# Kernel tuning notes

Measured on AMD Instinct MI355X. Metric: run time of the kernel, lower is better.

Reference implementation:

```python
import jax, jax.numpy as jnp
import numpy as np

CODE_NUM = 12288
GRAPH = 128      # graph_size: embedding width / GRU input
HIDDEN = 128     # GRU hidden = t_output_size = time_size (required by scatter/broadcast)
ATT = 64         # t_attention_size


def setup_inputs() -> dict:
    key = jax.random.key(0)
    ks = jax.random.split(key, 20)
    s = 0.05
    # disjoint 3-way membership masks (m1/m2/m3), some codes in no set
    cat = jax.random.randint(ks[0], (CODE_NUM,), 0, 4)
    divided = jax.nn.one_hot(cat, 4, dtype=jnp.int32)[:, :3]
    return {
        "interval": jnp.asarray(3.5, jnp.float32),
        "co_embeddings": jax.random.normal(ks[1], (CODE_NUM, GRAPH), jnp.float32),
        "no_embeddings": jax.random.normal(ks[2], (CODE_NUM, GRAPH), jnp.float32),
        "unrelated_embeddings": jax.random.normal(ks[3], (CODE_NUM, GRAPH), jnp.float32),
        "hidden_state": jax.random.normal(ks[4], (CODE_NUM, HIDDEN), jnp.float32),
        "divided": divided,
        # GRUCell params (torch layout: [3H, in], gates r|z|n)
        "W_ih": jax.random.normal(ks[5], (3 * HIDDEN, GRAPH), jnp.float32) * s,
        "W_hh": jax.random.normal(ks[6], (3 * HIDDEN, HIDDEN), jnp.float32) * s,
        "b_ih": jax.random.normal(ks[7], (3 * HIDDEN,), jnp.float32) * s,
        "b_hh": jax.random.normal(ks[8], (3 * HIDDEN,), jnp.float32) * s,
        # SingleHeadAttentionLayer params
        "Wq": jax.random.normal(ks[9], (ATT, GRAPH), jnp.float32) * s,
        "bq": jax.random.normal(ks[10], (ATT,), jnp.float32) * s,
        "Wk": jax.random.normal(ks[11], (ATT, GRAPH), jnp.float32) * s,
        "bk": jax.random.normal(ks[12], (ATT,), jnp.float32) * s,
        "Wv": jax.random.normal(ks[13], (HIDDEN, GRAPH), jnp.float32) * s,
        "bv": jax.random.normal(ks[14], (HIDDEN,), jnp.float32) * s,
        # time_layer: Linear(1, time_size)
        "Wt": jax.random.normal(ks[15], (HIDDEN, 1), jnp.float32) * s,
        "bt": jax.random.normal(ks[16], (HIDDEN,), jnp.float32) * s,
        "t": 1,
        "is_last": 0,
    }


def _gru_cell(x, h, W_ih, W_hh, b_ih, b_hh):
    gi = x @ W_ih.T + b_ih          # [N, 3H]
    gh = h @ W_hh.T + b_hh          # [N, 3H]
    i_r, i_z, i_n = jnp.split(gi, 3, axis=-1)
    h_r, h_z, h_n = jnp.split(gh, 3, axis=-1)
    r = jax.nn.sigmoid(i_r + h_r)
    z = jax.nn.sigmoid(i_z + h_z)
    n = jnp.tanh(i_n + r * h_n)
    return (1.0 - z) * n + z * h


def reference(interval, co_embeddings, no_embeddings, unrelated_embeddings,
              hidden_state, divided, W_ih, W_hh, b_ih, b_hh,
              Wq, bq, Wk, bk, Wv, bv, Wt, bt, t, is_last):
    dt = co_embeddings.dtype
    # time feature: tanh(Linear(1/log(interval + e)))
    x_t = 1.0 / jnp.log(interval + jnp.e)                       # scalar
    time_features = jnp.tanh(x_t * Wt[:, 0] + bt)               # [H]

    if is_last:
        out = _gru_cell(co_embeddings, hidden_state, W_ih, W_hh, b_ih, b_hh)
        return (out + time_features, None)

    m1 = divided[:, 0] > 0
    m2 = divided[:, 1] > 0
    m3 = divided[:, 2] > 0
    m23 = m2 | m3
    NEG = jnp.finfo(dt).min

    # --- m1 branch: GRUCell is row-wise, so compute on all rows and mask ---
    h_gru = _gru_cell(co_embeddings, hidden_state, W_ih, W_hh, b_ih, b_hh)  # [N, H]
    output_m1 = jnp.max(jnp.where(m1[:, None], h_gru, NEG), axis=0)        # [H]

    # --- m2/m3 branch: attention over the m23 subset (mask-based, order-free)
    # query rows: m2 -> no_embeddings, m3 -> unrelated_embeddings
    q_full = jnp.where(m2[:, None], no_embeddings, unrelated_embeddings)   # [N, G]
    Q = q_full @ Wq.T + bq                                                 # [N, A]
    K = co_embeddings @ Wk.T + bk                                          # [N, A]
    V = co_embeddings @ Wv.T + bv                                          # [N, H]
    scores = (Q @ K.T) / jnp.sqrt(jnp.asarray(ATT, dt))                    # [N, N]
    scores = jnp.where(m23[None, :], scores, NEG)                          # keys restricted to m23
    attn = jax.nn.softmax(scores, axis=-1)
    h_att = jnp.tanh(attn @ V)                                             # [N, H]
    output_m23 = jnp.max(jnp.where(m23[:, None], h_att, NEG), axis=0)      # [H]

    # scatter: m2/m3 rows written after m1 rows (m23 takes precedence)
    h_new = jnp.where(m23[:, None], h_att,
                      jnp.where(m1[:, None], h_gru, jnp.zeros((), dt)))

    output = jnp.maximum(output_m1, output_m23)
    return (output + time_features, h_new)
```

## Files before the change

### kernel.cpp

```cpp
#include <hip/hip_runtime.h>
#include <hip/hip_bf16.h>
#include <math.h>

#define N_CODES 12288
#define G 128
#define H 128
#define ATT 64
#define NEGF (-3.4028234663852886e38f)
#define NSEG 8
#define QT 64
#define NQT (N_CODES / QT)
#define QMAX 7168

typedef __attribute__((ext_vector_type(8))) short bf16x8;
typedef __attribute__((ext_vector_type(4))) float f32x4;
typedef __hip_bfloat16 bf16;
#define MFMA16(a, b, c) __builtin_amdgcn_mfma_f32_16x16x32_bf16(a, b, c, 0, 0, 0)

struct __align__(16) Ws {
  int n1;
  int n23;
  int pad_[2];
  int idx1[N_CODES];
  int rows23[N_CODES];
  int flags23[N_CODES];
  unsigned maxu[128];
  float tf[128];
  float lseg[NSEG * QMAX];
  float bqkv[256];
  float b2[512];
  bf16 Wqkv[16 * 4 * 64 * 8];
  bf16 W2[32 * 8 * 64 * 8];
  bf16 Qb[(size_t)N_CODES * ATT];
  bf16 Kf[(size_t)N_CODES * ATT];
  bf16 Vf[(size_t)N_CODES * H];
  bf16 Oseg[(size_t)NSEG * QMAX * H];
};

__device__ inline uint2 pack4(float4 v) {
  union { bf16 b[4]; uint2 u; } cv;
  cv.b[0] = __float2bfloat16(v.x);
  cv.b[1] = __float2bfloat16(v.y);
  cv.b[2] = __float2bfloat16(v.z);
  cv.b[3] = __float2bfloat16(v.w);
  return cv.u;
}

__device__ inline float bf2f(short s) {
  union { unsigned u; float f; } c;
  c.u = ((unsigned)(unsigned short)s) << 16;
  return c.f;
}

__device__ inline unsigned fkey(float f) {
  unsigned b = __float_as_uint(f);
  return (b & 0x80000000u) ? ~b : (b | 0x80000000u);
}
__device__ inline float funkey(unsigned u) {
  unsigned b = (u & 0x80000000u) ? (u & 0x7fffffffu) : ~u;
  return __uint_as_float(b);
}

__global__ void k_setup(const int* __restrict__ divided,
                        const float* __restrict__ Wq, const float* __restrict__ bq,
                        const float* __restrict__ Wk, const float* __restrict__ bk,
                        const float* __restrict__ Wv, const float* __restrict__ bv,
                        const float* __restrict__ W_ih, const float* __restrict__ W_hh,
                        const float* __restrict__ b_ih, const float* __restrict__ b_hh,
                        const float* __restrict__ interval, const float* __restrict__ Wt,
                        const float* __restrict__ bt, Ws* ws) {
  int bid = blockIdx.x;
  int t = threadIdx.x;
  if (bid < 48) {
    int r = bid * 256 + t;
    int m1 = divided[r * 3 + 0] > 0;
    int m2 = divided[r * 3 + 1] > 0;
    int m3 = divided[r * 3 + 2] > 0;
    if (m1) {
      int p = atomicAdd(&ws->n1, 1);
      ws->idx1[p] = r;
    }
    if (m2 | m3) {
      int p = atomicAdd(&ws->n23, 1);
      ws->rows23[p] = r;
      ws->flags23[p] = m2;
    }
    return;
  }
  if (bid < 176) {
    int idx = (bid - 48) * 256 + t;
    int c = idx >> 7, k = idx & 127;
    float v;
    if (c < 64) v = Wq[c * G + k] * 0.125f;
    else if (c < 128) v = Wk[(c - 64) * G + k];
    else v = Wv[(c - 128) * G + k];
    int NB = c >> 4, lo = c & 15, ks = k >> 5, hi = (k >> 3) & 3, j = k & 7;
    ws->Wqkv[((NB * 4 + ks) * 64 + hi * 16 + lo) * 8 + j] = __float2bfloat16(v);
    return;
  }
  if (bid < 688) {
    int idx = (bid - 176) * 256 + t;
    int c = idx >> 8, k = idx & 255;
    int g = c >> 7, d = c & 127;
    float v = 0.f;
    if (g == 0) v = (k < 128) ? W_ih[d * G + k] : W_hh[d * H + (k - 128)];
    else if (g == 1) v = (k < 128) ? W_ih[(128 + d) * G + k] : W_hh[(128 + d) * H + (k - 128)];
    else if (g == 2) v = (k < 128) ? W_ih[(256 + d) * G + k] : 0.f;
    else v = (k < 128) ? 0.f : W_hh[(256 + d) * H + (k - 128)];
    int NB = c >> 4, lo = c & 15, ks = k >> 5, hi = (k >> 3) & 3, j = k & 7;
    ws->W2[((NB * 8 + ks) * 64 + hi * 16 + lo) * 8 + j] = __float2bfloat16(v);
    return;
  }
  if (t < 128) {
    float xt = 1.0f / logf(interval[0] + 2.718281828459045f);
    ws->tf[t] = tanhf(xt * Wt[t] + bt[t]);
    ws->maxu[t] = 0u;
  }
  for (int i = t; i < 768; i += 256) {
    if (i < 256) {
      float v;
      if (i < 64) v = bq[i] * 0.125f;
      else if (i < 128) v = bk[i - 64];
      else v = bv[i - 128];
      ws->bqkv[i] = v;
    } else {
      int c = i - 256;
      int g = c >> 7, d = c & 127;
      float v;
      if (g == 0) v = b_ih[d] + b_hh[d];
      else if (g == 1) v = b_ih[128 + d] + b_hh[128 + d];
      else if (g == 2) v = b_ih[256 + d];
      else v = b_hh[256 + d];
      ws->b2[c] = v;
    }
  }
}

__launch_bounds__(256)
__global__ void k_mm(const float* __restrict__ co, const float* __restrict__ no_e,
                     const float* __restrict__ un_e, const float* __restrict__ hs,
                     Ws* ws, float* __restrict__ h_new) {
  __shared__ __align__(16) bf16 sm[8704];
  int bid = blockIdx.x;
  int t = threadIdx.x;
  int w = t >> 6, lane = t & 63, lo = lane & 15, hi = lane >> 4;

  if (bid < 384) {
    int n23 = ws->n23;
    int q0 = bid * 32;
    if (q0 >= n23) return;
    bf16(*Aq)[136] = (bf16(*)[136])sm;
    bf16(*Ac)[136] = (bf16(*)[136])(sm + 4352);
    for (int it = 0; it < 4; ++it) {
      int idx = it * 256 + t;
      int rr = idx >> 5, c4 = idx & 31;
      uint2 pq = {0, 0}, pc = {0, 0};
      int p = q0 + rr;
      if (p < n23) {
        int row = ws->rows23[p];
        const float* srcq = ws->flags23[p] ? no_e : un_e;
        pq = pack4(*(const float4*)&srcq[(size_t)row * G + c4 * 4]);
        pc = pack4(*(const float4*)&co[(size_t)row * G + c4 * 4]);
      }
      *(uint2*)&Aq[rr][c4 * 4] = pq;
      *(uint2*)&Ac[rr][c4 * 4] = pc;
    }
    __syncthreads();
    const bf16(*At)[136] = (w == 0) ? Aq : Ac;
    f32x4 acc[2][4];
#pragma unroll
    for (int mf = 0; mf < 2; ++mf)
#pragma unroll
      for (int nb = 0; nb < 4; ++nb) acc[mf][nb] = (f32x4){0.f, 0.f, 0.f, 0.f};
#pragma unroll
    for (int ks = 0; ks < 4; ++ks) {
      bf16x8 af0 = *(const bf16x8*)&At[lo][ks * 32 + hi * 8];
      bf16x8 af1 = *(const bf16x8*)&At[16 + lo][ks * 32 + hi * 8];
#pragma unroll
      for (int nb = 0; nb < 4; ++nb) {
        bf16x8 bfr = *(const bf16x8*)&ws->Wqkv[(((w * 4 + nb) * 4 + ks) * 64 + lane) * 8];
        acc[0][nb] = MFMA16(af0, bfr, acc[0][nb]);
        acc[1][nb] = MFMA16(af1, bfr, acc[1][nb]);
      }
    }
#pragma unroll
    for (int mf = 0; mf < 2; ++mf) {
#pragma unroll
      for (int nb = 0; nb < 4; ++nb) {
        int c = w * 64 + nb * 16 + lo;
        float bias = ws->bqkv[c];
#pragma unroll
        for (int r = 0; r < 4; ++r) {
          int p = q0 + mf * 16 + hi * 4 + r;
          if (p >= n23) continue;
          bf16 bv16 = __float2bfloat16(acc[mf][nb][r] + bias);
          if (c < 64) {
            ws->Qb[(size_t)p * ATT + c] = bv16;
          } else if (c < 128) {
            int d = c - 64;
            ws->Kf[(((p >> 4) * 2 + (d >> 5)) * 64 + ((d >> 3) & 3) * 16 + (p & 15)) * 8 + (d & 7)] = bv16;
          } else {
            int d = c - 128;
            ws->Vf[((((p >> 6) * 8 + (d >> 4)) * 2 + ((p >> 5) & 1)) * 64 + ((p >> 3) & 3) * 16 + (d & 15)) * 8 + (p & 7)] = bv16;
          }
        }
      }
    }
  } else {
    int n1 = ws->n1;
    int q0 = (bid - 384) * 32;
    if (q0 >= n1) return;
    bf16(*A2)[264] = (bf16(*)[264])sm;
    for (int it = 0; it < 8; ++it) {
      int idx = it * 256 + t;
      int rr = idx >> 6, c4 = idx & 63;
      uint2 pk = {0, 0};
      int p = q0 + rr;
      if (p < n1) {
        int row = ws->idx1[p];
        float4 v = (c4 < 32) ? *(const float4*)&co[(size_t)row * G + c4 * 4]
                             : *(const float4*)&hs[(size_t)row * H + (c4 - 32) * 4];
        pk = pack4(v);
      }
      *(uint2*)&A2[rr][c4 * 4] = pk;
    }
    __syncthreads();
    f32x4 acc[2][8];
#pragma unroll
    for (int mf = 0; mf < 2; ++mf)
#pragma unroll
      for (int x = 0; x < 8; ++x) acc[mf][x] = (f32x4){0.f, 0.f, 0.f, 0.f};
#pragma unroll
    for (int ks = 0; ks < 8; ++ks) {
      bf16x8 af0 = *(const bf16x8*)&A2[lo][ks * 32 + hi * 8];
      bf16x8 af1 = *(const bf16x8*)&A2[16 + lo][ks * 32 + hi * 8];
#pragma unroll
      for (int g = 0; g < 4; ++g) {
#pragma unroll
        for (int nb2 = 0; nb2 < 2; ++nb2) {
          int NB = g * 8 + w * 2 + nb2;
          bf16x8 bfr = *(const bf16x8*)&ws->W2[((NB * 8 + ks) * 64 + lane) * 8];
          acc[0][g * 2 + nb2] = MFMA16(af0, bfr, acc[0][g * 2 + nb2]);
          acc[1][g * 2 + nb2] = MFMA16(af1, bfr, acc[1][g * 2 + nb2]);
        }
      }
    }
    float mx2[2] = {NEGF, NEGF};
#pragma unroll
    for (int mf = 0; mf < 2; ++mf) {
#pragma unroll
      for (int nb2 = 0; nb2 < 2; ++nb2) {
        int d = w * 32 + nb2 * 16 + lo;
        float br = ws->b2[d], bz = ws->b2[128 + d], bin_ = ws->b2[256 + d], bhn = ws->b2[384 + d];
#pragma unroll
        for (int r = 0; r < 4; ++r) {
          int p = q0 + mf * 16 + hi * 4 + r;
          if (p >= n1) continue;
          int row = ws->idx1[p];
          float rs = acc[mf][0 + nb2][r] + br;
          float zs = acc[mf][2 + nb2][r] + bz;
          float in_ = acc[mf][4 + nb2][r] + bin_;
          float hn = acc[mf][6 + nb2][r] + bhn;
          float rg = 1.f / (1.f + __expf(-rs));
          float zg = 1.f / (1.f + __expf(-zs));
          float ng = tanhf(in_ + rg * hn);
          float h0 = hs[(size_t)row * H + d];
          float hv = (1.f - zg) * ng + zg * h0;
          h_new[(size_t)row * H + d] = hv;
          mx2[nb2] = fmaxf(mx2[nb2], hv);
        }
      }
    }
#pragma unroll
    for (int nb2 = 0; nb2 < 2; ++nb2) {
      float m = mx2[nb2];
      m = fmaxf(m, __shfl_xor(m, 16));
      m = fmaxf(m, __shfl_xor(m, 32));
      if (hi == 0) atomicMax(&ws->maxu[w * 32 + nb2 * 16 + lo], fkey(m));
    }
  }
}

__launch_bounds__(256)
__global__ void k_attn(const Ws* __restrict__ ws, Ws* __restrict__ wso) {
  int n23 = ws->n23;
  int bid = blockIdx.x;
  int q0 = (bid % NQT) * QT;
  int seg = bid / NQT;
  if (q0 >= n23) return;
  int segk = (((n23 + NSEG - 1) / NSEG) + 63) & ~63;
  int s0 = seg * segk;
  int t = threadIdx.x;
  if (s0 >= n23) {
    for (int idx = t; idx < QT * 32; idx += 256) {
      int q = q0 + (idx >> 5);
      if (q < n23) {
        uint2 z2 = {0, 0};
        *(uint2*)&wso->Oseg[((size_t)seg * QMAX + q) * H + (idx & 31) * 4] = z2;
      }
    }
    if (t < QT && q0 + t < n23) wso->lseg[seg * QMAX + q0 + t] = 0.f;
    return;
  }
  int send = min(s0 + segk, n23);

  int w = t >> 6, lane = t & 63, lo = lane & 15, hi = lane >> 4;

  __shared__ bf16 Pl[64][72];

  bf16x8 qf[4][2];
#pragma unroll
  for (int qsub = 0; qsub < 4; ++qsub)
#pragma unroll
    for (int s = 0; s < 2; ++s)
      qf[qsub][s] =
          *(const bf16x8*)&ws->Qb[(size_t)(q0 + qsub * 16 + lo) * ATT + s * 32 + hi * 8];

  f32x4 acc[2][4];
#pragma unroll
  for (int ddl = 0; ddl < 2; ++ddl)
#pragma unroll
    for (int qsub = 0; qsub < 4; ++qsub) acc[ddl][qsub] = (f32x4){0.f, 0.f, 0.f, 0.f};
  float lacc = 0.f;

  for (int c0 = s0; c0 < send; c0 += 64) {
    int kb = (c0 >> 4) + w;
    bf16x8 kf0 = *(const bf16x8*)&ws->Kf[((size_t)(kb * 2 + 0) * 64 + lane) * 8];
    bf16x8 kf1 = *(const bf16x8*)&ws->Kf[((size_t)(kb * 2 + 1) * 64 + lane) * 8];
    bool kv = (c0 + w * 16 + lo) < send;
#pragma unroll
    for (int qsub = 0; qsub < 4; ++qsub) {
      f32x4 s_ = {0.f, 0.f, 0.f, 0.f};
      s_ = MFMA16(qf[qsub][0], kf0, s_);
      s_ = MFMA16(qf[qsub][1], kf1, s_);
#pragma unroll
      for (int r = 0; r < 4; ++r) {
        float p = kv ? __expf(s_[r]) : 0.f;
        Pl[qsub * 16 + hi * 4 + r][w * 16 + lo] = __float2bfloat16(p);
      }
    }
    __syncthreads();

    int kc = c0 >> 6;
#pragma unroll
    for (int s = 0; s < 2; ++s) {
      bf16x8 pf[4];
#pragma unroll
      for (int qsub = 0; qsub < 4; ++qsub)
        pf[qsub] = *(const bf16x8*)&Pl[qsub * 16 + lo][s * 32 + hi * 8];
#pragma unroll
      for (int ddl = 0; ddl < 2; ++ddl) {
        bf16x8 vf =
            *(const bf16x8*)&ws->Vf[((size_t)(kc * 16 + (w * 2 + ddl) * 2 + s) * 64 + lane) * 8];
#pragma unroll
        for (int qsub = 0; qsub < 4; ++qsub) acc[ddl][qsub] = MFMA16(vf, pf[qsub], acc[ddl][qsub]);
      }
    }
    {
      bf16x8 pa = *(const bf16x8*)&Pl[w * 16 + lo][hi * 16];
      bf16x8 pb = *(const bf16x8*)&Pl[w * 16 + lo][hi * 16 + 8];
      float sl = 0.f;
#pragma unroll
      for (int j = 0; j < 8; ++j) sl += bf2f(pa[j]) + bf2f(pb[j]);
      sl += __shfl_xor(sl, 16);
      sl += __shfl_xor(sl, 32);
      lacc += sl;
    }
    __syncthreads();
  }

  if (hi == 0) {
    int q = q0 + w * 16 + lo;
    if (q < n23) wso->lseg[seg * QMAX + q] = lacc;
  }
#pragma unroll
  for (int qsub = 0; qsub < 4; ++qsub) {
    int q = q0 + qsub * 16 + lo;
    if (q < n23) {
#pragma unroll
      for (int ddl = 0; ddl < 2; ++ddl) {
        union { bf16 b[4]; uint2 u; } tmp;
#pragma unroll
        for (int r = 0; r < 4; ++r) tmp.b[r] = __float2bfloat16(acc[ddl][qsub][r]);
        *(uint2*)&wso->Oseg[((size_t)seg * QMAX + q) * H + w * 32 + ddl * 16 + hi * 4] = tmp.u;
      }
    }
  }
}

__global__ void k_merge(const Ws* __restrict__ ws, float* __restrict__ h_new, Ws* wso) {
  int n23 = ws->n23;
  int qb = blockIdx.x * 32;
  if (qb >= n23) return;
  int t = threadIdx.x;
  int d = t & 127, half = t >> 7;
  float mx = NEGF;
  for (int qi = 0; qi < 16; ++qi) {
    int q = qb + half * 16 + qi;
    if (q >= n23) break;
    float o = 0.f, L = 0.f;
#pragma unroll
    for (int s = 0; s < NSEG; ++s) {
      o += bf2f(((const short*)ws->Oseg)[((size_t)s * QMAX + q) * H + d]);
      L += ws->lseg[s * QMAX + q];
    }
    float h = tanhf(o / L);
    h_new[(size_t)ws->rows23[q] * H + d] = h;
    mx = fmaxf(mx, h);
  }
  __shared__ float red[256];
  red[t] = mx;
  __syncthreads();
  if (t < 128) atomicMax(&wso->maxu[t], fkey(fmaxf(red[t], red[t + 128])));
}

__global__ void k_final(const Ws* __restrict__ ws, float* __restrict__ out) {
  int h = threadIdx.x;
  out[h] = funkey(ws->maxu[h]) + ws->tf[h];
}

extern "C" void kernel_launch(void* const* d_in, const int* in_sizes, int n_in,
                              void* d_out, int out_size, void* d_ws, size_t ws_size,
                              hipStream_t stream) {
  const float* interval = (const float*)d_in[0];
  const float* co = (const float*)d_in[1];
  const float* no_e = (const float*)d_in[2];
  const float* un_e = (const float*)d_in[3];
  const float* hs = (const float*)d_in[4];
  const int* divided = (const int*)d_in[5];
  const float* W_ih = (const float*)d_in[6];
  const float* W_hh = (const float*)d_in[7];
  const float* b_ih = (const float*)d_in[8];
  const float* b_hh = (const float*)d_in[9];
  const float* Wq = (const float*)d_in[10];
  const float* bq = (const float*)d_in[11];
  const float* Wk = (const float*)d_in[12];
  const float* bk = (const float*)d_in[13];
  const float* Wv = (const float*)d_in[14];
  const float* bv = (const float*)d_in[15];
  const float* Wt = (const float*)d_in[16];
  const float* bt = (const float*)d_in[17];

  float* out = (float*)d_out;
  float* h_new = out + 128;
  Ws* ws = (Ws*)d_ws;

  hipMemsetAsync(d_out, 0, (size_t)out_size * sizeof(float), stream);
  hipMemsetAsync(ws, 0, 16, stream);

  k_setup<<<689, 256, 0, stream>>>(divided, Wq, bq, Wk, bk, Wv, bv, W_ih, W_hh, b_ih, b_hh,
                                   interval, Wt, bt, ws);
  k_mm<<<768, 256, 0, stream>>>(co, no_e, un_e, hs, ws, h_new);
  k_attn<<<NQT * NSEG, 256, 0, stream>>>(ws, ws);
  k_merge<<<QMAX / 32, 256, 0, stream>>>(ws, h_new, ws);
  k_final<<<1, 128, 0, stream>>>(ws, out);
}
```

Measured before the change: 194.6 us.

## Vectorize weight packing, shrink matmul tiles, fuse final reduction into merge

The weight-repacking setup blocks now read float4 and write packed bf16 quads, which cuts the setup grid from 689 to 209 blocks. The projection and GRU matmul blocks drop from 32 to 16 rows so more blocks share the work. The attention grid is sized by QMAX instead of N_CODES so fewer blocks exit early. Attention now computes the transposed score tile, so P is stored as packed 64-bit writes and the row sums are accumulated in registers, removing the extra LDS re-read. The k_final launch is folded into k_merge through a last-block counter, which adds a threadfence and atomic handshake.

```diff
diff --git a/kernel.cpp b/kernel.cpp
--- a/kernel.cpp
+++ b/kernel.cpp
@@ -9,8 +9,8 @@
 #define NEGF (-3.4028234663852886e38f)
 #define NSEG 8
 #define QT 64
-#define NQT (N_CODES / QT)
 #define QMAX 7168
+#define NQTA (QMAX / QT)
 
 typedef __attribute__((ext_vector_type(8))) short bf16x8;
 typedef __attribute__((ext_vector_type(4))) float f32x4;
@@ -20,7 +20,8 @@
 struct __align__(16) Ws {
   int n1;
   int n23;
-  int pad_[2];
+  int cnt;
+  int pad_;
   int idx1[N_CODES];
   int rows23[N_CODES];
   int flags23[N_CODES];
@@ -87,28 +88,35 @@
     }
     return;
   }
-  if (bid < 176) {
+  if (bid < 80) {
     int idx = (bid - 48) * 256 + t;
-    int c = idx >> 7, k = idx & 127;
-    float v;
-    if (c < 64) v = Wq[c * G + k] * 0.125f;
-    else if (c < 128) v = Wk[(c - 64) * G + k];
-    else v = Wv[(c - 128) * G + k];
+    int c = idx >> 5, k = (idx & 31) * 4;
+    float4 v;
+    if (c < 64) {
+      v = *(const float4*)&Wq[c * G + k];
+      v.x *= 0.125f; v.y *= 0.125f; v.z *= 0.125f; v.w *= 0.125f;
+    } else if (c < 128) {
+      v = *(const float4*)&Wk[(c - 64) * G + k];
+    } else {
+      v = *(const float4*)&Wv[(c - 128) * G + k];
+    }
     int NB = c >> 4, lo = c & 15, ks = k >> 5, hi = (k >> 3) & 3, j = k & 7;
-    ws->Wqkv[((NB * 4 + ks) * 64 + hi * 16 + lo) * 8 + j] = __float2bfloat16(v);
+    *(uint2*)&ws->Wqkv[((NB * 4 + ks) * 64 + hi * 16 + lo) * 8 + j] = pack4(v);
     return;
   }
-  if (bid < 688) {
-    int idx = (bid - 176) * 256 + t;
-    int c = idx >> 8, k = idx & 255;
+  if (bid < 208) {
+    int idx = (bid - 80) * 256 + t;
+    int c = idx >> 6, k = (idx & 63) * 4;
     int g = c >> 7, d = c & 127;
-    float v = 0.f;
-    if (g == 0) v = (k < 128) ? W_ih[d * G + k] : W_hh[d * H + (k - 128)];
-    else if (g == 1) v = (k < 128) ? W_ih[(128 + d) * G + k] : W_hh[(128 + d) * H + (k - 128)];
-    else if (g == 2) v = (k < 128) ? W_ih[(256 + d) * G + k] : 0.f;
-    else v = (k < 128) ? 0.f : W_hh[(256 + d) * H + (k - 128)];
+    float4 v = {0.f, 0.f, 0.f, 0.f};
+    if (g == 0) v = (k < 128) ? *(const float4*)&W_ih[d * G + k]
+                              : *(const float4*)&W_hh[d * H + (k - 128)];
+    else if (g == 1) v = (k < 128) ? *(const float4*)&W_ih[(128 + d) * G + k]
+                                   : *(const float4*)&W_hh[(128 + d) * H + (k - 128)];
+    else if (g == 2) { if (k < 128) v = *(const float4*)&W_ih[(256 + d) * G + k]; }
+    else { if (k >= 128) v = *(const float4*)&W_hh[(256 + d) * H + (k - 128)]; }
     int NB = c >> 4, lo = c & 15, ks = k >> 5, hi = (k >> 3) & 3, j = k & 7;
-    ws->W2[((NB * 8 + ks) * 64 + hi * 16 + lo) * 8 + j] = __float2bfloat16(v);
+    *(uint2*)&ws->W2[((NB * 8 + ks) * 64 + hi * 16 + lo) * 8 + j] = pack4(v);
     return;
   }
   if (t < 128) {
@@ -145,13 +153,13 @@
   int t = threadIdx.x;
   int w = t >> 6, lane = t & 63, lo = lane & 15, hi = lane >> 4;
 
-  if (bid < 384) {
+  if (bid < 448) {
     int n23 = ws->n23;
-    int q0 = bid * 32;
+    int q0 = bid * 16;
     if (q0 >= n23) return;
     bf16(*Aq)[136] = (bf16(*)[136])sm;
-    bf16(*Ac)[136] = (bf16(*)[136])(sm + 4352);
-    for (int it = 0; it < 4; ++it) {
+    bf16(*Ac)[136] = (bf16(*)[136])(sm + 2176);
+    for (int it = 0; it < 2; ++it) {
       int idx = it * 256 + t;
       int rr = idx >> 5, c4 = idx & 31;
       uint2 pq = {0, 0}, pc = {0, 0};
@@ -167,51 +175,44 @@
     }
     __syncthreads();
     const bf16(*At)[136] = (w == 0) ? Aq : Ac;
-    f32x4 acc[2][4];
-#pragma unroll
-    for (int mf = 0; mf < 2; ++mf)
-#pragma unroll
-      for (int nb = 0; nb < 4; ++nb) acc[mf][nb] = (f32x4){0.f, 0.f, 0.f, 0.f};
+    f32x4 acc[4];
+#pragma unroll
+    for (int nb = 0; nb < 4; ++nb) acc[nb] = (f32x4){0.f, 0.f, 0.f, 0.f};
 #pragma unroll
     for (int ks = 0; ks < 4; ++ks) {
-      bf16x8 af0 = *(const bf16x8*)&At[lo][ks * 32 + hi * 8];
-      bf16x8 af1 = *(const bf16x8*)&At[16 + lo][ks * 32 + hi * 8];
+      bf16x8 af = *(const bf16x8*)&At[lo][ks * 32 + hi * 8];
 #pragma unroll
       for (int nb = 0; nb < 4; ++nb) {
         bf16x8 bfr = *(const bf16x8*)&ws->Wqkv[(((w * 4 + nb) * 4 + ks) * 64 + lane) * 8];
-        acc[0][nb] = MFMA16(af0, bfr, acc[0][nb]);
-        acc[1][nb] = MFMA16(af1, bfr, acc[1][nb]);
-      }
-    }
-#pragma unroll
-    for (int mf = 0; mf < 2; ++mf) {
-#pragma unroll
-      for (int nb = 0; nb < 4; ++nb) {
-        int c = w * 64 + nb * 16 + lo;
-        float bias = ws->bqkv[c];
-#pragma unroll
-        for (int r = 0; r < 4; ++r) {
-          int p = q0 + mf * 16 + hi * 4 + r;
-          if (p >= n23) continue;
-          bf16 bv16 = __float2bfloat16(acc[mf][nb][r] + bias);
-          if (c < 64) {
-            ws->Qb[(size_t)p * ATT + c] = bv16;
-          } else if (c < 128) {
-            int d = c - 64;
-            ws->Kf[(((p >> 4) * 2 + (d >> 5)) * 64 + ((d >> 3) & 3) * 16 + (p & 15)) * 8 + (d & 7)] = bv16;
-          } else {
-            int d = c - 128;
-            ws->Vf[((((p >> 6) * 8 + (d >> 4)) * 2 + ((p >> 5) & 1)) * 64 + ((p >> 3) & 3) * 16 + (d & 15)) * 8 + (p & 7)] = bv16;
-          }
+        acc[nb] = MFMA16(af, bfr, acc[nb]);
+      }
+    }
+#pragma unroll
+    for (int nb = 0; nb < 4; ++nb) {
+      int c = w * 64 + nb * 16 + lo;
+      float bias = ws->bqkv[c];
+#pragma unroll
+      for (int r = 0; r < 4; ++r) {
+        int p = q0 + hi * 4 + r;
+        if (p >= n23) continue;
+        bf16 bv16 = __float2bfloat16(acc[nb][r] + bias);
+        if (c < 64) {
+          ws->Qb[(size_t)p * ATT + c] = bv16;
+        } else if (c < 128) {
+          int d = c - 64;
+          ws->Kf[(((p >> 4) * 2 + (d >> 5)) * 64 + ((d >> 3) & 3) * 16 + (p & 15)) * 8 + (d & 7)] = bv16;
+        } else {
+          int d = c - 128;
+          ws->Vf[((((p >> 6) * 8 + (d >> 4)) * 2 + ((p >> 5) & 1)) * 64 + ((p >> 3) & 3) * 16 + (d & 15)) * 8 + (p & 7)] = bv16;
         }
       }
     }
   } else {
     int n1 = ws->n1;
-    int q0 = (bid - 384) * 32;
+    int q0 = (bid - 448) * 16;
     if (q0 >= n1) return;
     bf16(*A2)[264] = (bf16(*)[264])sm;
-    for (int it = 0; it < 8; ++it) {
+    for (int it = 0; it < 4; ++it) {
       int idx = it * 256 + t;
       int rr = idx >> 6, c4 = idx & 63;
       uint2 pk = {0, 0};
@@ -225,50 +226,43 @@
       *(uint2*)&A2[rr][c4 * 4] = pk;
     }
     __syncthreads();
-    f32x4 acc[2][8];
-#pragma unroll
-    for (int mf = 0; mf < 2; ++mf)
-#pragma unroll
-      for (int x = 0; x < 8; ++x) acc[mf][x] = (f32x4){0.f, 0.f, 0.f, 0.f};
+    f32x4 acc[8];
+#pragma unroll
+    for (int x = 0; x < 8; ++x) acc[x] = (f32x4){0.f, 0.f, 0.f, 0.f};
 #pragma unroll
     for (int ks = 0; ks < 8; ++ks) {
-      bf16x8 af0 = *(const bf16x8*)&A2[lo][ks * 32 + hi * 8];
-      bf16x8 af1 = *(const bf16x8*)&A2[16 + lo][ks * 32 + hi * 8];
+      bf16x8 af = *(const bf16x8*)&A2[lo][ks * 32 + hi * 8];
 #pragma unroll
       for (int g = 0; g < 4; ++g) {
 #pragma unroll
         for (int nb2 = 0; nb2 < 2; ++nb2) {
           int NB = g * 8 + w * 2 + nb2;
           bf16x8 bfr = *(const bf16x8*)&ws->W2[((NB * 8 + ks) * 64 + lane) * 8];
-          acc[0][g * 2 + nb2] = MFMA16(af0, bfr, acc[0][g * 2 + nb2]);
-          acc[1][g * 2 + nb2] = MFMA16(af1, bfr, acc[1][g * 2 + nb2]);
+          acc[g * 2 + nb2] = MFMA16(af, bfr, acc[g * 2 + nb2]);
         }
       }
     }
     float mx2[2] = {NEGF, NEGF};
 #pragma unroll
-    for (int mf = 0; mf < 2; ++mf) {
-#pragma unroll
-      for (int nb2 = 0; nb2 < 2; ++nb2) {
-        int d = w * 32 + nb2 * 16 + lo;
-        float br = ws->b2[d], bz = ws->b2[128 + d], bin_ = ws->b2[256 + d], bhn = ws->b2[384 + d];
-#pragma unroll
-        for (int r = 0; r < 4; ++r) {
-          int p = q0 + mf * 16 + hi * 4 + r;
-          if (p >= n1) continue;
-          int row = ws->idx1[p];
-          float rs = acc[mf][0 + nb2][r] + br;
-          float zs = acc[mf][2 + nb2][r] + bz;
-          float in_ = acc[mf][4 + nb2][r] + bin_;
-          float hn = acc[mf][6 + nb2][r] + bhn;
-          float rg = 1.f / (1.f + __expf(-rs));
-          float zg = 1.f / (1.f + __expf(-zs));
-          float ng = tanhf(in_ + rg * hn);
-          float h0 = hs[(size_t)row * H + d];
-          float hv = (1.f - zg) * ng + zg * h0;
-          h_new[(size_t)row * H + d] = hv;
-          mx2[nb2] = fmaxf(mx2[nb2], hv);
-        }
+    for (int nb2 = 0; nb2 < 2; ++nb2) {
+      int d = w * 32 + nb2 * 16 + lo;
+      float br = ws->b2[d], bz = ws->b2[128 + d], bin_ = ws->b2[256 + d], bhn = ws->b2[384 + d];
+#pragma unroll
+      for (int r = 0; r < 4; ++r) {
+        int p = q0 + hi * 4 + r;
+        if (p >= n1) continue;
+        int row = ws->idx1[p];
+        float rs = acc[0 + nb2][r] + br;
+        float zs = acc[2 + nb2][r] + bz;
+        float in_ = acc[4 + nb2][r] + bin_;
+        float hn = acc[6 + nb2][r] + bhn;
+        float rg = 1.f / (1.f + __expf(-rs));
+        float zg = 1.f / (1.f + __expf(-zs));
+        float ng = tanhf(in_ + rg * hn);
+        float h0 = hs[(size_t)row * H + d];
+        float hv = (1.f - zg) * ng + zg * h0;
+        h_new[(size_t)row * H + d] = hv;
+        mx2[nb2] = fmaxf(mx2[nb2], hv);
       }
     }
 #pragma unroll
@@ -285,8 +279,8 @@
 __global__ void k_attn(const Ws* __restrict__ ws, Ws* __restrict__ wso) {
   int n23 = ws->n23;
   int bid = blockIdx.x;
-  int q0 = (bid % NQT) * QT;
-  int seg = bid / NQT;
+  int q0 = (bid % NQTA) * QT;
+  int seg = bid / NQTA;
   if (q0 >= n23) return;
   int segk = (((n23 + NSEG - 1) / NSEG) + 63) & ~63;
   int s0 = seg * segk;
@@ -307,6 +301,7 @@
   int w = t >> 6, lane = t & 63, lo = lane & 15, hi = lane >> 4;
 
   __shared__ bf16 Pl[64][72];
+  __shared__ float Lw[4][64];
 
   bf16x8 qf[4][2];
 #pragma unroll
@@ -321,23 +316,30 @@
   for (int ddl = 0; ddl < 2; ++ddl)
 #pragma unroll
     for (int qsub = 0; qsub < 4; ++qsub) acc[ddl][qsub] = (f32x4){0.f, 0.f, 0.f, 0.f};
-  float lacc = 0.f;
+  float lacc[4] = {0.f, 0.f, 0.f, 0.f};
 
   for (int c0 = s0; c0 < send; c0 += 64) {
     int kb = (c0 >> 4) + w;
     bf16x8 kf0 = *(const bf16x8*)&ws->Kf[((size_t)(kb * 2 + 0) * 64 + lane) * 8];
     bf16x8 kf1 = *(const bf16x8*)&ws->Kf[((size_t)(kb * 2 + 1) * 64 + lane) * 8];
-    bool kv = (c0 + w * 16 + lo) < send;
 #pragma unroll
     for (int qsub = 0; qsub < 4; ++qsub) {
       f32x4 s_ = {0.f, 0.f, 0.f, 0.f};
-      s_ = MFMA16(qf[qsub][0], kf0, s_);
-      s_ = MFMA16(qf[qsub][1], kf1, s_);
+      s_ = MFMA16(kf0, qf[qsub][0], s_);
+      s_ = MFMA16(kf1, qf[qsub][1], s_);
+      union { bf16 b[4]; uint2 u; } tu;
+      float sl = 0.f;
 #pragma unroll
       for (int r = 0; r < 4; ++r) {
-        float p = kv ? __expf(s_[r]) : 0.f;
-        Pl[qsub * 16 + hi * 4 + r][w * 16 + lo] = __float2bfloat16(p);
-      }
+        int key = c0 + w * 16 + hi * 4 + r;
+        float p = (key < send) ? __expf(s_[r]) : 0.f;
+        sl += p;
+        tu.b[r] = __float2bfloat16(p);
+      }
+      *(uint2*)&Pl[qsub * 16 + lo][w * 16 + hi * 4] = tu.u;
+      sl += __shfl_xor(sl, 16);
+      sl += __shfl_xor(sl, 32);
+      lacc[qsub] += sl;
     }
     __syncthreads();
 
@@ -356,22 +358,17 @@
         for (int qsub = 0; qsub < 4; ++qsub) acc[ddl][qsub] = MFMA16(vf, pf[qsub], acc[ddl][qsub]);
       }
     }
-    {
-      bf16x8 pa = *(const bf16x8*)&Pl[w * 16 + lo][hi * 16];
-      bf16x8 pb = *(const bf16x8*)&Pl[w * 16 + lo][hi * 16 + 8];
-      float sl = 0.f;
-#pragma unroll
-      for (int j = 0; j < 8; ++j) sl += bf2f(pa[j]) + bf2f(pb[j]);
-      sl += __shfl_xor(sl, 16);
-      sl += __shfl_xor(sl, 32);
-      lacc += sl;
-    }
     __syncthreads();
   }
 
   if (hi == 0) {
-    int q = q0 + w * 16 + lo;
-    if (q < n23) wso->lseg[seg * QMAX + q] = lacc;
+#pragma unroll
+    for (int qsub = 0; qsub < 4; ++qsub) Lw[w][qsub * 16 + lo] = lacc[qsub];
+  }
+  __syncthreads();
+  if (t < QT) {
+    int q = q0 + t;
+    if (q < n23) wso->lseg[seg * QMAX + q] = Lw[0][t] + Lw[1][t] + Lw[2][t] + Lw[3][t];
   }
 #pragma unroll
   for (int qsub = 0; qsub < 4; ++qsub) {
@@ -388,7 +385,8 @@
   }
 }
 
-__global__ void k_merge(const Ws* __restrict__ ws, float* __restrict__ h_new, Ws* wso) {
+__global__ void k_merge(const Ws* __restrict__ ws, float* __restrict__ h_new, Ws* wso,
+                        float* __restrict__ out) {
   int n23 = ws->n23;
   int qb = blockIdx.x * 32;
   if (qb >= n23) return;
@@ -409,14 +407,21 @@
     mx = fmaxf(mx, h);
   }
   __shared__ float red[256];
+  __shared__ int lastv;
   red[t] = mx;
   __syncthreads();
   if (t < 128) atomicMax(&wso->maxu[t], fkey(fmaxf(red[t], red[t + 128])));
-}
-
-__global__ void k_final(const Ws* __restrict__ ws, float* __restrict__ out) {
-  int h = threadIdx.x;
-  out[h] = funkey(ws->maxu[h]) + ws->tf[h];
+  __syncthreads();
+  if (t == 0) {
+    __threadfence();
+    int nact = (n23 + 31) >> 5;
+    lastv = (atomicAdd(&wso->cnt, 1) == nact - 1) ? 1 : 0;
+  }
+  __syncthreads();
+  if (lastv && t < 128) {
+    unsigned u = atomicOr(&wso->maxu[t], 0u);
+    out[t] = funkey(u) + ws->tf[t];
+  }
 }
 
 extern "C" void kernel_launch(void* const* d_in, const int* in_sizes, int n_in,
@@ -448,10 +453,9 @@
   hipMemsetAsync(d_out, 0, (size_t)out_size * sizeof(float), stream);
   hipMemsetAsync(ws, 0, 16, stream);
 
-  k_setup<<<689, 256, 0, stream>>>(divided, Wq, bq, Wk, bk, Wv, bv, W_ih, W_hh, b_ih, b_hh,
+  k_setup<<<209, 256, 0, stream>>>(divided, Wq, bq, Wk, bk, Wv, bv, W_ih, W_hh, b_ih, b_hh,
                                    interval, Wt, bt, ws);
-  k_mm<<<768, 256, 0, stream>>>(co, no_e, un_e, hs, ws, h_new);
-  k_attn<<<NQT * NSEG, 256, 0, stream>>>(ws, ws);
-  k_merge<<<QMAX / 32, 256, 0, stream>>>(ws, h_new, ws);
-  k_final<<<1, 128, 0, stream>>>(ws, out);
-}
+  k_mm<<<704, 256, 0, stream>>>(co, no_e, un_e, hs, ws, h_new);
+  k_attn<<<NQTA * NSEG, 256, 0, stream>>>(ws, ws);
+  k_merge<<<QMAX / 32, 256, 0, stream>>>(ws, h_new, ws, out);
+}
```

Result: faster. 190.2 us (-2.3%).
